# Optimization experiments

Hardware: AMD Instinct MI355X
Metric: run time of the kernel (lower is better)

The kernel has to match this reference:

```python
import jax, jax.numpy as jnp
import numpy as np
from jax.scipy.special import logsumexp

SPARSITY = 0.0


def setup_inputs() -> dict:
    key = jax.random.key(0)
    k1, k2, k3, k4, k5 = jax.random.split(key, 5)
    N, M = 65536, 1024
    sample = jax.random.uniform(k1, (N, 2), dtype=jnp.float32)
    mu = jax.random.uniform(k2, (M, 2), dtype=jnp.float32)
    sigma_log = jax.random.uniform(k3, (M, 2), dtype=jnp.float32)
    theta = jax.random.normal(k4, (M,), dtype=jnp.float32)
    w = jax.random.normal(k5, (M, 1), dtype=jnp.float32)
    return {"sample": sample, "mu": mu, "sigma_log": sigma_log, "theta": theta, "w": w}


def reference(sample, mu, sigma_log, theta, w):
    # Anisotropic covariance entries: gamma_j = R(theta)^T diag(sig2) R(theta)
    sig2 = jnp.exp(-2.0 * sigma_log)            # [M,2], inverse variances
    a, b = sig2[:, 0], sig2[:, 1]
    c, s = jnp.cos(theta), jnp.sin(theta)
    g11 = a * c**2 + b * s**2                   # [M]
    g12 = (a - b) * c * s                       # [M]
    g22 = a * s**2 + b * c**2                   # [M]

    # Log weights: log_softmax(w) - sum(sigma_log) (normalization factor)
    wlog = jax.nn.log_softmax(w, axis=0)[:, 0] - sigma_log.sum(axis=1)  # [M]

    # All-pairs anisotropic quadratic form, fused per-coordinate (no [N,M,2] tensor)
    dx = sample[:, None, 0] - mu[None, :, 0]    # [N,M]
    dy = sample[:, None, 1] - mu[None, :, 1]    # [N,M]
    qf = g11 * dx * dx + 2.0 * g12 * dx * dy + g22 * dy * dy  # [N,M]

    # Log-density at each sample: logsumexp over mixture components
    ll = logsumexp(wlog[None, :] - qf, axis=1)  # [N]

    # Negative log-likelihood + sparsity penalty
    nll = -ll.sum() + SPARSITY * jnp.sqrt(jax.nn.softmax(w, axis=0)).sum()
    return nll
```

## Files before the change

### kernel.cpp

```cpp
#include <hip/hip_runtime.h>
#include <math.h>

#define LOG2E 1.4426950408889634f
#define LN2   0.6931471805599453f

typedef float v2f __attribute__((ext_vector_type(2)));

__global__ __launch_bounds__(1024) void gm_fused(
    const float* __restrict__ sample,
    const float* __restrict__ mu,
    const float* __restrict__ sigma_log,
    const float* __restrict__ theta,
    const float* __restrict__ w,
    float* __restrict__ out,
    int M)
{
    __shared__ float4 recs4[512 * 3];
    __shared__ float  ws[16];
    __shared__ float  psum[16][64];

    const int tid  = threadIdx.x;
    const int lane = tid & 63;
    const int wid  = tid >> 6;

    const int i = blockIdx.x * 64 + lane;
    const float2 sv = ((const float2*)sample)[i];

    const float wj = w[tid];
    float e = __expf(wj);
    #pragma unroll
    for (int off = 32; off > 0; off >>= 1)
        e += __shfl_down(e, off, 64);
    if (lane == 0) ws[wid] = e;
    __syncthreads();
    float tot = 0.0f;
    #pragma unroll
    for (int k = 0; k < 16; ++k) tot += ws[k];
    const float lse = __logf(tot);

    {
        const float sl0 = sigma_log[2 * tid + 0];
        const float sl1 = sigma_log[2 * tid + 1];
        const float a = __expf(-2.0f * sl0);
        const float b = __expf(-2.0f * sl1);
        const float th = theta[tid];
        const float c = __cosf(th);
        const float s = __sinf(th);

        const float g11 = a * c * c + b * s * s;
        const float g12 = (a - b) * c * s;
        const float g22 = a * s * s + b * c * c;

        const float mx = mu[2 * tid + 0];
        const float my = mu[2 * tid + 1];

        const float wlog = wj - lse - (sl0 + sl1);

        const float A = g11;
        const float B = 2.0f * g12;
        const float C = g22;
        const float D = -(2.0f * g11 * mx + 2.0f * g12 * my);
        const float E = -(2.0f * g12 * mx + 2.0f * g22 * my);
        const float F = g11 * mx * mx + 2.0f * g12 * mx * my + g22 * my * my;
        const float K = (wlog - F) * LOG2E;

        float* recs = (float*)recs4;
        const int base = 12 * (tid >> 1) + (tid & 1);
        recs[base + 0]  = -A * LOG2E;
        recs[base + 2]  = -B * LOG2E;
        recs[base + 4]  = -C * LOG2E;
        recs[base + 6]  = -D * LOG2E;
        recs[base + 8]  = -E * LOG2E;
        recs[base + 10] = K;
    }
    __syncthreads();

    const float sx = sv.x, sy = sv.y;
    const v2f xx2 = (v2f)(sx * sx);
    const v2f xy2 = (v2f)(sx * sy);
    const v2f yy2 = (v2f)(sy * sy);
    const v2f sx2 = (v2f)(sx);
    const v2f sy2 = (v2f)(sy);

    const int pairs = M >> 5;
    const int p0 = wid * pairs;

    v2f acc[4];
    #pragma unroll
    for (int u = 0; u < 4; ++u) acc[u] = (v2f)(0.0f);

    for (int p = 0; p < pairs; p += 4) {
        #pragma unroll
        for (int u = 0; u < 4; ++u) {
            const float4* r4 = &recs4[3 * (p0 + p + u)];
            const float4 r0 = r4[0];
            const float4 r1 = r4[1];
            const float4 r2 = r4[2];
            const v2f ra = {r0.x, r0.y};
            const v2f rb = {r0.z, r0.w};
            const v2f rc = {r1.x, r1.y};
            const v2f rd = {r1.z, r1.w};
            const v2f re = {r2.x, r2.y};
            const v2f rk = {r2.z, r2.w};

            v2f ev = rk;
            ev = __builtin_elementwise_fma(ra, xx2, ev);
            ev = __builtin_elementwise_fma(rb, xy2, ev);
            ev = __builtin_elementwise_fma(rc, yy2, ev);
            ev = __builtin_elementwise_fma(rd, sx2, ev);
            ev = __builtin_elementwise_fma(re, sy2, ev);

            v2f ex;
            ex.x = __builtin_amdgcn_exp2f(ev.x);
            ex.y = __builtin_amdgcn_exp2f(ev.y);
            acc[u] += ex;
        }
    }

    const v2f accv = (acc[0] + acc[1]) + (acc[2] + acc[3]);
    psum[wid][lane] = accv.x + accv.y;
    __syncthreads();

    if (tid < 64) {
        float t = 0.0f;
        #pragma unroll
        for (int k = 0; k < 16; ++k) t += psum[k][tid];
        float v = -LN2 * __builtin_amdgcn_logf(t);
        #pragma unroll
        for (int off = 32; off > 0; off >>= 1)
            v += __shfl_down(v, off, 64);
        if (tid == 0) atomicAdd(out, v);
    }
}

extern "C" void kernel_launch(void* const* d_in, const int* in_sizes, int n_in,
                              void* d_out, int out_size, void* d_ws, size_t ws_size,
                              hipStream_t stream) {
    const float* sample    = (const float*)d_in[0];
    const float* mu        = (const float*)d_in[1];
    const float* sigma_log = (const float*)d_in[2];
    const float* theta     = (const float*)d_in[3];
    const float* w         = (const float*)d_in[4];
    float* out = (float*)d_out;

    const int M = in_sizes[3];
    const int N = in_sizes[0] / 2;

    hipMemsetAsync(out, 0, sizeof(float), stream);

    const int grid = N / 64;
    gm_fused<<<grid, 1024, 0, stream>>>(sample, mu, sigma_log, theta, w, out, M);
}
```

Before: 80.35 us.

## Process four samples per thread so each LDS record load serves four samples

Each thread now handles four samples instead of one, and every block covers 256 samples, so the grid is four times smaller. Each component record read from LDS is reused across four sample evaluations. This cuts LDS traffic per exp and amortizes the per-block precompute of component coefficients and the log-softmax over four times as many samples. The cost is more registers per thread and fewer blocks (256), which may leave compute units underfilled on a large GPU.

```diff
diff --git a/kernel.cpp b/kernel.cpp
--- a/kernel.cpp
+++ b/kernel.cpp
@@ -17,14 +17,19 @@
 {
     __shared__ float4 recs4[512 * 3];
     __shared__ float  ws[16];
-    __shared__ float  psum[16][64];
+    __shared__ float  psum[16][256];
+    __shared__ float  bsum[4];
 
     const int tid  = threadIdx.x;
     const int lane = tid & 63;
     const int wid  = tid >> 6;
 
-    const int i = blockIdx.x * 64 + lane;
-    const float2 sv = ((const float2*)sample)[i];
+    const int ib = blockIdx.x * 256;
+    const float2* sam = (const float2*)sample;
+    const float2 sv0 = sam[ib + lane];
+    const float2 sv1 = sam[ib + lane + 64];
+    const float2 sv2 = sam[ib + lane + 128];
+    const float2 sv3 = sam[ib + lane + 192];
 
     const float wj = w[tid];
     float e = __expf(wj);
@@ -75,23 +80,27 @@
     }
     __syncthreads();
 
-    const float sx = sv.x, sy = sv.y;
-    const v2f xx2 = (v2f)(sx * sx);
-    const v2f xy2 = (v2f)(sx * sy);
-    const v2f yy2 = (v2f)(sy * sy);
-    const v2f sx2 = (v2f)(sx);
-    const v2f sy2 = (v2f)(sy);
+    #define FEAT(svN, xxN, xyN, yyN, sxN, syN)                 \
+        const v2f xxN = (v2f)(svN.x * svN.x);                  \
+        const v2f xyN = (v2f)(svN.x * svN.y);                  \
+        const v2f yyN = (v2f)(svN.y * svN.y);                  \
+        const v2f sxN = (v2f)(svN.x);                          \
+        const v2f syN = (v2f)(svN.y);
+    FEAT(sv0, xx0, xy0, yy0, sx0, sy0)
+    FEAT(sv1, xx1, xy1, yy1, sx1, sy1)
+    FEAT(sv2, xx2, xy2, yy2, sx2, sy2)
+    FEAT(sv3, xx3, xy3, yy3, sx3, sy3)
+    #undef FEAT
 
     const int pairs = M >> 5;
     const int p0 = wid * pairs;
 
-    v2f acc[4];
-    #pragma unroll
-    for (int u = 0; u < 4; ++u) acc[u] = (v2f)(0.0f);
+    v2f acc0 = (v2f)(0.0f), acc1 = (v2f)(0.0f);
+    v2f acc2 = (v2f)(0.0f), acc3 = (v2f)(0.0f);
 
-    for (int p = 0; p < pairs; p += 4) {
+    for (int p = 0; p < pairs; p += 2) {
         #pragma unroll
-        for (int u = 0; u < 4; ++u) {
+        for (int u = 0; u < 2; ++u) {
             const float4* r4 = &recs4[3 * (p0 + p + u)];
             const float4 r0 = r4[0];
             const float4 r1 = r4[1];
@@ -103,25 +112,34 @@
             const v2f re = {r2.x, r2.y};
             const v2f rk = {r2.z, r2.w};
 
-            v2f ev = rk;
-            ev = __builtin_elementwise_fma(ra, xx2, ev);
-            ev = __builtin_elementwise_fma(rb, xy2, ev);
-            ev = __builtin_elementwise_fma(rc, yy2, ev);
-            ev = __builtin_elementwise_fma(rd, sx2, ev);
-            ev = __builtin_elementwise_fma(re, sy2, ev);
-
-            v2f ex;
-            ex.x = __builtin_amdgcn_exp2f(ev.x);
-            ex.y = __builtin_amdgcn_exp2f(ev.y);
-            acc[u] += ex;
+            #define BODY(xxN, xyN, yyN, sxN, syN, accN)        \
+            {                                                  \
+                v2f ev = rk;                                   \
+                ev = __builtin_elementwise_fma(ra, xxN, ev);   \
+                ev = __builtin_elementwise_fma(rb, xyN, ev);   \
+                ev = __builtin_elementwise_fma(rc, yyN, ev);   \
+                ev = __builtin_elementwise_fma(rd, sxN, ev);   \
+                ev = __builtin_elementwise_fma(re, syN, ev);   \
+                v2f ex;                                        \
+                ex.x = __builtin_amdgcn_exp2f(ev.x);           \
+                ex.y = __builtin_amdgcn_exp2f(ev.y);           \
+                accN += ex;                                    \
+            }
+            BODY(xx0, xy0, yy0, sx0, sy0, acc0)
+            BODY(xx1, xy1, yy1, sx1, sy1, acc1)
+            BODY(xx2, xy2, yy2, sx2, sy2, acc2)
+            BODY(xx3, xy3, yy3, sx3, sy3, acc3)
+            #undef BODY
         }
     }
 
-    const v2f accv = (acc[0] + acc[1]) + (acc[2] + acc[3]);
-    psum[wid][lane] = accv.x + accv.y;
+    psum[wid][lane]       = acc0.x + acc0.y;
+    psum[wid][lane + 64]  = acc1.x + acc1.y;
+    psum[wid][lane + 128] = acc2.x + acc2.y;
+    psum[wid][lane + 192] = acc3.x + acc3.y;
     __syncthreads();
 
-    if (tid < 64) {
+    if (tid < 256) {
         float t = 0.0f;
         #pragma unroll
         for (int k = 0; k < 16; ++k) t += psum[k][tid];
@@ -129,8 +147,11 @@
         #pragma unroll
         for (int off = 32; off > 0; off >>= 1)
             v += __shfl_down(v, off, 64);
-        if (tid == 0) atomicAdd(out, v);
+        if ((tid & 63) == 0) bsum[tid >> 6] = v;
     }
+    __syncthreads();
+    if (tid == 0)
+        atomicAdd(out, (bsum[0] + bsum[1]) + (bsum[2] + bsum[3]));
 }
 
 extern "C" void kernel_launch(void* const* d_in, const int* in_sizes, int n_in,
@@ -148,6 +169,6 @@
 
     hipMemsetAsync(out, 0, sizeof(float), stream);
 
-    const int grid = N / 64;
+    const int grid = N / 256;
     gm_fused<<<grid, 1024, 0, stream>>>(sample, mu, sigma_log, theta, w, out, M);
 }
```

Result: faster. 77.35 us (-3.7%).

## Split mixture components across blocks and register-tile eight samples per thread

Applied to the files above, without the earlier changes.

Each block now handles 512 samples against half of the mixture components. Every thread keeps 8 samples in registers and reuses each LDS record load across those 8 samples. This cuts LDS traffic per exp and amortizes the per-block component preprocessing over more samples. Partial sums go to a workspace buffer, and a second kernel combines the two halves, takes the log and reduces. The cost is an extra kernel launch, a global round-trip for the partials, and more register pressure.

```diff
diff --git a/kernel.cpp b/kernel.cpp
--- a/kernel.cpp
+++ b/kernel.cpp
@@ -6,25 +6,39 @@
 
 typedef float v2f __attribute__((ext_vector_type(2)));
 
-__global__ __launch_bounds__(1024) void gm_fused(
+__global__ __launch_bounds__(1024) void gm_pass1(
     const float* __restrict__ sample,
     const float* __restrict__ mu,
     const float* __restrict__ sigma_log,
     const float* __restrict__ theta,
     const float* __restrict__ w,
-    float* __restrict__ out,
-    int M)
+    float* __restrict__ part,
+    int N, int M)
 {
-    __shared__ float4 recs4[512 * 3];
+    __shared__ float4 recs4[256 * 3];
     __shared__ float  ws[16];
-    __shared__ float  psum[16][64];
+    __shared__ float  psum[16][512];
 
     const int tid  = threadIdx.x;
     const int lane = tid & 63;
     const int wid  = tid >> 6;
 
-    const int i = blockIdx.x * 64 + lane;
-    const float2 sv = ((const float2*)sample)[i];
+    const int half = blockIdx.x & 1;
+    const int sg   = blockIdx.x >> 1;
+    const int s0g  = sg * 512;
+    const int m0   = half * (M >> 1);
+
+    const float2* sam = (const float2*)sample;
+    float fxx[8], fxy[8], fyy[8], fsx[8], fsy[8];
+    #pragma unroll
+    for (int s = 0; s < 8; ++s) {
+        const float2 sv = sam[s0g + lane + 64 * s];
+        fxx[s] = sv.x * sv.x;
+        fxy[s] = sv.x * sv.y;
+        fyy[s] = sv.y * sv.y;
+        fsx[s] = sv.x;
+        fsy[s] = sv.y;
+    }
 
     const float wj = w[tid];
     float e = __expf(wj);
@@ -38,12 +52,14 @@
     for (int k = 0; k < 16; ++k) tot += ws[k];
     const float lse = __logf(tot);
 
-    {
-        const float sl0 = sigma_log[2 * tid + 0];
-        const float sl1 = sigma_log[2 * tid + 1];
+    if (tid < (M >> 1)) {
+        const int j = m0 + tid;
+        const float wjj = w[j];
+        const float sl0 = sigma_log[2 * j + 0];
+        const float sl1 = sigma_log[2 * j + 1];
         const float a = __expf(-2.0f * sl0);
         const float b = __expf(-2.0f * sl1);
-        const float th = theta[tid];
+        const float th = theta[j];
         const float c = __cosf(th);
         const float s = __sinf(th);
 
@@ -51,10 +67,10 @@
         const float g12 = (a - b) * c * s;
         const float g22 = a * s * s + b * c * c;
 
-        const float mx = mu[2 * tid + 0];
-        const float my = mu[2 * tid + 1];
+        const float mx = mu[2 * j + 0];
+        const float my = mu[2 * j + 1];
 
-        const float wlog = wj - lse - (sl0 + sl1);
+        const float wlog = wjj - lse - (sl0 + sl1);
 
         const float A = g11;
         const float B = 2.0f * g12;
@@ -75,61 +91,75 @@
     }
     __syncthreads();
 
-    const float sx = sv.x, sy = sv.y;
-    const v2f xx2 = (v2f)(sx * sx);
-    const v2f xy2 = (v2f)(sx * sy);
-    const v2f yy2 = (v2f)(sy * sy);
-    const v2f sx2 = (v2f)(sx);
-    const v2f sy2 = (v2f)(sy);
+    const int p0 = wid * 16;
 
-    const int pairs = M >> 5;
-    const int p0 = wid * pairs;
+    v2f acc[8];
+    #pragma unroll
+    for (int s = 0; s < 8; ++s) acc[s] = (v2f)(0.0f);
 
-    v2f acc[4];
-    #pragma unroll
-    for (int u = 0; u < 4; ++u) acc[u] = (v2f)(0.0f);
+    for (int p = 0; p < 16; ++p) {
+        const float4* r4 = &recs4[3 * (p0 + p)];
+        const float4 r0 = r4[0];
+        const float4 r1 = r4[1];
+        const float4 r2 = r4[2];
+        const v2f ra = {r0.x, r0.y};
+        const v2f rb = {r0.z, r0.w};
+        const v2f rc = {r1.x, r1.y};
+        const v2f rd = {r1.z, r1.w};
+        const v2f re = {r2.x, r2.y};
+        const v2f rk = {r2.z, r2.w};
 
-    for (int p = 0; p < pairs; p += 4) {
         #pragma unroll
-        for (int u = 0; u < 4; ++u) {
-            const float4* r4 = &recs4[3 * (p0 + p + u)];
-            const float4 r0 = r4[0];
-            const float4 r1 = r4[1];
-            const float4 r2 = r4[2];
-            const v2f ra = {r0.x, r0.y};
-            const v2f rb = {r0.z, r0.w};
-            const v2f rc = {r1.x, r1.y};
-            const v2f rd = {r1.z, r1.w};
-            const v2f re = {r2.x, r2.y};
-            const v2f rk = {r2.z, r2.w};
-
+        for (int s = 0; s < 8; ++s) {
             v2f ev = rk;
-            ev = __builtin_elementwise_fma(ra, xx2, ev);
-            ev = __builtin_elementwise_fma(rb, xy2, ev);
-            ev = __builtin_elementwise_fma(rc, yy2, ev);
-            ev = __builtin_elementwise_fma(rd, sx2, ev);
-            ev = __builtin_elementwise_fma(re, sy2, ev);
-
+            ev = __builtin_elementwise_fma(ra, (v2f)(fxx[s]), ev);
+            ev = __builtin_elementwise_fma(rb, (v2f)(fxy[s]), ev);
+            ev = __builtin_elementwise_fma(rc, (v2f)(fyy[s]), ev);
+            ev = __builtin_elementwise_fma(rd, (v2f)(fsx[s]), ev);
+            ev = __builtin_elementwise_fma(re, (v2f)(fsy[s]), ev);
             v2f ex;
             ex.x = __builtin_amdgcn_exp2f(ev.x);
             ex.y = __builtin_amdgcn_exp2f(ev.y);
-            acc[u] += ex;
+            acc[s] += ex;
         }
     }
 
-    const v2f accv = (acc[0] + acc[1]) + (acc[2] + acc[3]);
-    psum[wid][lane] = accv.x + accv.y;
+    #pragma unroll
+    for (int s = 0; s < 8; ++s)
+        psum[wid][lane + 64 * s] = acc[s].x + acc[s].y;
     __syncthreads();
 
-    if (tid < 64) {
+    if (tid < 512) {
         float t = 0.0f;
         #pragma unroll
         for (int k = 0; k < 16; ++k) t += psum[k][tid];
-        float v = -LN2 * __builtin_amdgcn_logf(t);
+        part[half * N + s0g + tid] = t;
+    }
+}
+
+__global__ __launch_bounds__(1024) void gm_pass2(
+    const float* __restrict__ part,
+    float* __restrict__ out,
+    int N)
+{
+    const int i = blockIdx.x * 1024 + threadIdx.x;
+    const float t = part[i] + part[N + i];
+    float v = -LN2 * __builtin_amdgcn_logf(t);
+
+    #pragma unroll
+    for (int off = 32; off > 0; off >>= 1)
+        v += __shfl_down(v, off, 64);
+
+    __shared__ float bs[16];
+    const int lane = threadIdx.x & 63;
+    const int wid  = threadIdx.x >> 6;
+    if (lane == 0) bs[wid] = v;
+    __syncthreads();
+    if (threadIdx.x == 0) {
+        float t2 = 0.0f;
         #pragma unroll
-        for (int off = 32; off > 0; off >>= 1)
-            v += __shfl_down(v, off, 64);
-        if (tid == 0) atomicAdd(out, v);
+        for (int k = 0; k < 16; ++k) t2 += bs[k];
+        atomicAdd(out, t2);
     }
 }
 
@@ -141,13 +171,18 @@
     const float* sigma_log = (const float*)d_in[2];
     const float* theta     = (const float*)d_in[3];
     const float* w         = (const float*)d_in[4];
-    float* out = (float*)d_out;
+    float* out  = (float*)d_out;
+    float* part = (float*)d_ws;
 
     const int M = in_sizes[3];
     const int N = in_sizes[0] / 2;
 
     hipMemsetAsync(out, 0, sizeof(float), stream);
 
-    const int grid = N / 64;
-    gm_fused<<<grid, 1024, 0, stream>>>(sample, mu, sigma_log, theta, w, out, M);
+    const int grid1 = (N / 512) * 2;
+    gm_pass1<<<grid1, 1024, 0, stream>>>(sample, mu, sigma_log, theta, w,
+                                         part, N, M);
+
+    const int grid2 = N / 1024;
+    gm_pass2<<<grid2, 1024, 0, stream>>>(part, out, N);
 }
```

Measured after the change: 79.31 us. No clear change (-1.3%).

## Compute quadratic forms via bf16 MFMA with hi/lo split-precision emulation

Applied to the files above, without the earlier changes.

Rewrites the per-pair quadratic form as a K=32 bf16 matrix product between sample feature vectors and per-component coefficients. Each fp32 value is split into bf16 hi and lo parts, and three cross terms are kept to approximate fp32 accuracy. The exp2 and sum over components run on the MFMA output, with a DPP row reduction. Each block now handles 256 samples instead of 64, which spreads the per-block parameter preprocessing over more samples. The costs are some precision loss from dropping the lo*lo term and a larger shared-memory footprint that may cut occupancy.

```diff
diff --git a/kernel.cpp b/kernel.cpp
--- a/kernel.cpp
+++ b/kernel.cpp
@@ -4,9 +4,25 @@
 #define LOG2E 1.4426950408889634f
 #define LN2   0.6931471805599453f
 
-typedef float v2f __attribute__((ext_vector_type(2)));
+typedef short bf8 __attribute__((ext_vector_type(8)));
+typedef float f4  __attribute__((ext_vector_type(4)));
 
-__global__ __launch_bounds__(1024) void gm_fused(
+__device__ __forceinline__ unsigned short bf_hi(float x) {
+    unsigned u = __float_as_uint(x);
+    return (unsigned short)((u + 0x7FFFu + ((u >> 16) & 1u)) >> 16);
+}
+
+#define DPP_ADD(x, ctrl) \
+    x += __int_as_float(__builtin_amdgcn_update_dpp(0, __float_as_int(x), ctrl, 0xF, 0xF, false))
+__device__ __forceinline__ float row_sum16(float x) {
+    DPP_ADD(x, 0x111);
+    DPP_ADD(x, 0x112);
+    DPP_ADD(x, 0x114);
+    DPP_ADD(x, 0x118);
+    return x;
+}
+
+__global__ __launch_bounds__(1024) void gm_mfma(
     const float* __restrict__ sample,
     const float* __restrict__ mu,
     const float* __restrict__ sigma_log,
@@ -15,16 +31,17 @@
     float* __restrict__ out,
     int M)
 {
-    __shared__ float4 recs4[512 * 3];
-    __shared__ float  ws[16];
-    __shared__ float  psum[16][64];
+    __shared__ __align__(16) unsigned short wrec[1024 * 40];
+    __shared__ __align__(16) unsigned short srec[256 * 40];
+    __shared__ float ws[16];
+    __shared__ float psum[16 * 256];
+    __shared__ float bsum[4];
 
     const int tid  = threadIdx.x;
     const int lane = tid & 63;
     const int wid  = tid >> 6;
-
-    const int i = blockIdx.x * 64 + lane;
-    const float2 sv = ((const float2*)sample)[i];
+    const int quad = lane >> 4;
+    const int col  = lane & 15;
 
     const float wj = w[tid];
     float e = __expf(wj);
@@ -56,81 +73,96 @@
 
         const float wlog = wj - lse - (sl0 + sl1);
 
-        const float A = g11;
-        const float B = 2.0f * g12;
-        const float C = g22;
-        const float D = -(2.0f * g11 * mx + 2.0f * g12 * my);
-        const float E = -(2.0f * g12 * mx + 2.0f * g22 * my);
+        float cf[6];
+        cf[0] = -g11 * LOG2E;
+        cf[1] = -2.0f * g12 * LOG2E;
+        cf[2] = -g22 * LOG2E;
+        cf[3] = 2.0f * (g11 * mx + g12 * my) * LOG2E;
+        cf[4] = 2.0f * (g12 * mx + g22 * my) * LOG2E;
         const float F = g11 * mx * mx + 2.0f * g12 * mx * my + g22 * my * my;
-        const float K = (wlog - F) * LOG2E;
+        cf[5] = (wlog - F) * LOG2E;
 
-        float* recs = (float*)recs4;
-        const int base = 12 * (tid >> 1) + (tid & 1);
-        recs[base + 0]  = -A * LOG2E;
-        recs[base + 2]  = -B * LOG2E;
-        recs[base + 4]  = -C * LOG2E;
-        recs[base + 6]  = -D * LOG2E;
-        recs[base + 8]  = -E * LOG2E;
-        recs[base + 10] = K;
+        unsigned short r[32];
+        #pragma unroll
+        for (int s2 = 0; s2 < 6; ++s2) {
+            const unsigned short h = bf_hi(cf[s2]);
+            const float hf = __uint_as_float((unsigned)h << 16);
+            const unsigned short l = bf_hi(cf[s2] - hf);
+            r[s2] = h; r[6 + s2] = l; r[12 + s2] = h;
+        }
+        #pragma unroll
+        for (int s2 = 18; s2 < 32; ++s2) r[s2] = 0;
+        unsigned* dst = (unsigned*)&wrec[tid * 40];
+        #pragma unroll
+        for (int k = 0; k < 16; ++k)
+            dst[k] = ((unsigned)r[2 * k + 1] << 16) | r[2 * k];
+    }
+
+    if (tid < 256) {
+        const float2 sv = ((const float2*)sample)[blockIdx.x * 256 + tid];
+        float f[6];
+        f[0] = sv.x * sv.x; f[1] = sv.x * sv.y; f[2] = sv.y * sv.y;
+        f[3] = sv.x; f[4] = sv.y; f[5] = 1.0f;
+
+        unsigned short r[32];
+        #pragma unroll
+        for (int s2 = 0; s2 < 6; ++s2) {
+            const unsigned short h = bf_hi(f[s2]);
+            const float hf = __uint_as_float((unsigned)h << 16);
+            const unsigned short l = bf_hi(f[s2] - hf);
+            r[s2] = h; r[6 + s2] = h; r[12 + s2] = l;
+        }
+        #pragma unroll
+        for (int s2 = 18; s2 < 32; ++s2) r[s2] = 0;
+        unsigned* dst = (unsigned*)&srec[tid * 40];
+        #pragma unroll
+        for (int k = 0; k < 16; ++k)
+            dst[k] = ((unsigned)r[2 * k + 1] << 16) | r[2 * k];
     }
     __syncthreads();
 
-    const float sx = sv.x, sy = sv.y;
-    const v2f xx2 = (v2f)(sx * sx);
-    const v2f xy2 = (v2f)(sx * sy);
-    const v2f yy2 = (v2f)(sy * sy);
-    const v2f sx2 = (v2f)(sx);
-    const v2f sy2 = (v2f)(sy);
+    bf8 bfrag[4];
+    #pragma unroll
+    for (int ct = 0; ct < 4; ++ct) {
+        const int comp = wid * 64 + ct * 16 + col;
+        bfrag[ct] = *(const bf8*)&wrec[comp * 40 + quad * 8];
+    }
 
-    const int pairs = M >> 5;
-    const int p0 = wid * pairs;
-
-    v2f acc[4];
-    #pragma unroll
-    for (int u = 0; u < 4; ++u) acc[u] = (v2f)(0.0f);
-
-    for (int p = 0; p < pairs; p += 4) {
+    const f4 zero = {0.0f, 0.0f, 0.0f, 0.0f};
+    for (int st = 0; st < 16; ++st) {
+        const bf8 afrag = *(const bf8*)&srec[(st * 16 + col) * 40 + quad * 8];
+        float a0 = 0.0f, a1 = 0.0f, a2 = 0.0f, a3 = 0.0f;
         #pragma unroll
-        for (int u = 0; u < 4; ++u) {
-            const float4* r4 = &recs4[3 * (p0 + p + u)];
-            const float4 r0 = r4[0];
-            const float4 r1 = r4[1];
-            const float4 r2 = r4[2];
-            const v2f ra = {r0.x, r0.y};
-            const v2f rb = {r0.z, r0.w};
-            const v2f rc = {r1.x, r1.y};
-            const v2f rd = {r1.z, r1.w};
-            const v2f re = {r2.x, r2.y};
-            const v2f rk = {r2.z, r2.w};
-
-            v2f ev = rk;
-            ev = __builtin_elementwise_fma(ra, xx2, ev);
-            ev = __builtin_elementwise_fma(rb, xy2, ev);
-            ev = __builtin_elementwise_fma(rc, yy2, ev);
-            ev = __builtin_elementwise_fma(rd, sx2, ev);
-            ev = __builtin_elementwise_fma(re, sy2, ev);
-
-            v2f ex;
-            ex.x = __builtin_amdgcn_exp2f(ev.x);
-            ex.y = __builtin_amdgcn_exp2f(ev.y);
-            acc[u] += ex;
+        for (int ct = 0; ct < 4; ++ct) {
+            const f4 d = __builtin_amdgcn_mfma_f32_16x16x32_bf16(
+                afrag, bfrag[ct], zero, 0, 0, 0);
+            a0 += __builtin_amdgcn_exp2f(d[0]);
+            a1 += __builtin_amdgcn_exp2f(d[1]);
+            a2 += __builtin_amdgcn_exp2f(d[2]);
+            a3 += __builtin_amdgcn_exp2f(d[3]);
+        }
+        a0 = row_sum16(a0); a1 = row_sum16(a1);
+        a2 = row_sum16(a2); a3 = row_sum16(a3);
+        if (col == 15) {
+            f4 o = {a0, a1, a2, a3};
+            *(f4*)&psum[wid * 256 + st * 16 + quad * 4] = o;
         }
     }
-
-    const v2f accv = (acc[0] + acc[1]) + (acc[2] + acc[3]);
-    psum[wid][lane] = accv.x + accv.y;
     __syncthreads();
 
-    if (tid < 64) {
+    if (tid < 256) {
         float t = 0.0f;
         #pragma unroll
-        for (int k = 0; k < 16; ++k) t += psum[k][tid];
+        for (int k = 0; k < 16; ++k) t += psum[k * 256 + tid];
         float v = -LN2 * __builtin_amdgcn_logf(t);
         #pragma unroll
         for (int off = 32; off > 0; off >>= 1)
             v += __shfl_down(v, off, 64);
-        if (tid == 0) atomicAdd(out, v);
+        if ((tid & 63) == 0) bsum[tid >> 6] = v;
     }
+    __syncthreads();
+    if (tid == 0)
+        atomicAdd(out, (bsum[0] + bsum[1]) + (bsum[2] + bsum[3]));
 }
 
 extern "C" void kernel_launch(void* const* d_in, const int* in_sizes, int n_in,
@@ -148,6 +180,6 @@
 
     hipMemsetAsync(out, 0, sizeof(float), stream);
 
-    const int grid = N / 64;
-    gm_fused<<<grid, 1024, 0, stream>>>(sample, mu, sigma_log, theta, w, out, M);
+    const int grid = N / 256;
+    gm_mfma<<<grid, 1024, 0, stream>>>(sample, mu, sigma_log, theta, w, out, M);
 }
```

Measured after the change: 77.07 us. -4.1%, faster.
